# Optimization experiments

Measured on AMD Instinct MI355X. Metric: run time of the kernel, lower is better.

Reference implementation:

```python
import jax, jax.numpy as jnp
import numpy as np

MARGIN = 0.3
EPS = 1e-12


def setup_inputs() -> dict:
    key = jax.random.key(0)
    k1, k2, k3, k4 = jax.random.split(key, 4)
    B, N, D = 4, 6400, 32
    pred_masks = jax.random.normal(k1, (B, N, D), dtype=jnp.float32)
    pos_rand = jax.random.uniform(k2, (B, N), dtype=jnp.float32)
    target_gt_idx = jax.random.randint(k3, (B, N), 0, 20, dtype=jnp.int64)
    fg_mask = jax.random.randint(k4, (B, N), 0, 2) > 0
    return {
        "pred_masks": pred_masks,
        "pos_rand": pos_rand,
        "target_gt_idx": target_gt_idx,
        "fg_mask": fg_mask,
    }


def reference(pred_masks, pos_rand, target_gt_idx, fg_mask):
    B, N, D = pred_masks.shape
    # L2-normalize coefficients (F.normalize, eps=1e-12)
    norm = jnp.sqrt(jnp.sum(pred_masks * pred_masks, axis=-1, keepdims=True))
    coeffs = pred_masks / jnp.maximum(norm, EPS)  # [B,N,D]

    valid_pair = fg_mask[:, :, None] & fg_mask[:, None, :]  # [B,N,N]
    same_inst = target_gt_idx[:, :, None] == target_gt_idx[:, None, :]
    eye = jnp.eye(N, dtype=bool)
    S = valid_pair & same_inst & ~eye          # positives (same instance, not self)
    Dm = valid_pair & ~same_inst               # negatives (different instance)

    # Cosine similarities (vectors are unit norm)
    sims = jnp.einsum('bnd,bmd->bnm', coeffs, coeffs)  # [B,N,N]

    # Hardest negative per anchor: argmax similarity among negatives
    neg_idx = jnp.argmax(jnp.where(Dm, sims, -jnp.inf), axis=-1)  # [B,N]
    neg_vec = jnp.take_along_axis(coeffs, neg_idx[..., None], axis=1)  # [B,N,D]

    # Random positive: pick the k-th positive in anchor order, k = floor(u*num_pos)
    num_pos = jnp.sum(S, axis=-1)  # [B,N]
    pos_choice = jnp.floor(pos_rand * num_pos.astype(pos_rand.dtype)).astype(jnp.int32)
    pos_choice = jnp.clip(pos_choice, 0, jnp.maximum(num_pos - 1, 0).astype(jnp.int32))
    cum = jnp.cumsum(S.astype(jnp.int32), axis=-1)  # rank of each positive
    sel = S & (cum == (pos_choice + 1)[..., None])  # one-hot over chosen positive
    pos_idx = jnp.argmax(sel, axis=-1)  # [B,N]
    pos_vec = jnp.take_along_axis(coeffs, pos_idx[..., None], axis=1)  # [B,N,D]

    pos_d = jnp.sqrt(jnp.sum((coeffs - pos_vec) ** 2, axis=-1) + EPS)
    neg_d = jnp.sqrt(jnp.sum((coeffs - neg_vec) ** 2, axis=-1) + EPS)

    valid = fg_mask & (num_pos >= 1) & jnp.any(Dm, axis=-1)  # anchor forms a triplet
    per_anchor = jnp.maximum(pos_d - neg_d + MARGIN, 0.0)
    n_trip = jnp.sum(valid)
    total = jnp.sum(per_anchor * valid.astype(per_anchor.dtype))
    return jnp.where(n_trip > 0, total / jnp.maximum(n_trip, 1).astype(total.dtype), 0.0)
```

## Files before the change

### kernel.cpp

```cpp
#include <hip/hip_runtime.h>
#include <math.h>

#define B_ 4
#define N_ 6400
#define D_ 32
#define TJ 256
#define NCHJ 25
#define TI 128
#define CHUNK 256
#define NCC 25

typedef __attribute__((ext_vector_type(4))) float f32x4;
typedef __attribute__((ext_vector_type(8))) short bf16x8;

static constexpr float MARGIN_ = 0.3f;

__device__ __forceinline__ unsigned fmap(float f) {
    unsigned u = __float_as_uint(f);
    return (u & 0x80000000u) ? ~u : (u | 0x80000000u);
}
__device__ __forceinline__ float funmap(unsigned u) {
    return (u & 0x80000000u) ? __uint_as_float(u ^ 0x80000000u)
                             : __uint_as_float(~u);
}
#define NEG_INF_MAPPED 0x007FFFFFu

__device__ __forceinline__ unsigned short f2bf(float f) {
    unsigned u = __float_as_uint(f);
    unsigned r = u + 0x7fffu + ((u >> 16) & 1u);
    return (unsigned short)(r >> 16);
}
__device__ __forceinline__ float bf2f(unsigned short h) {
    return __uint_as_float(((unsigned)h) << 16);
}
__device__ __forceinline__ void bf2x(unsigned u, float& e0, float& e1) {
    e0 = __uint_as_float(u << 16);
    e1 = __uint_as_float(u & 0xffff0000u);
}

__global__ __launch_bounds__(256) void k_prep(const float* __restrict__ pred,
                                              const int* __restrict__ gt,
                                              const int* __restrict__ fg,
                                              unsigned short* __restrict__ hi_g,
                                              unsigned short* __restrict__ lo_g,
                                              int* __restrict__ clist,
                                              int* __restrict__ cg,
                                              int* __restrict__ Marr,
                                              unsigned* __restrict__ bestArr) {
    int c = blockIdx.x, b = blockIdx.y;
    int t = threadIdx.x;
    int lane = t & 63, w = t >> 6;
    int idx = c * CHUNK + t;

    bestArr[b * N_ + idx] = NEG_INF_MAPPED;

    bool flag = fg[b * N_ + idx] != 0;
    unsigned long long m = __ballot(flag);
    int lp = __popcll(m & ((1ull << lane) - 1ull));
    __shared__ int wsh[4];
    __shared__ int s_off, s_M;
    if (lane == 0) wsh[w] = __popcll(m);

    if (w == 0) {
        int pre = 0, tot = 0;
        #pragma unroll
        for (int cc = 0; cc < NCC; ++cc) {
            const int4 v = ((const int4*)(fg + (size_t)b * N_ + cc * CHUNK))[lane];
            int cnt = (v.x != 0) + (v.y != 0) + (v.z != 0) + (v.w != 0);
            #pragma unroll
            for (int o = 1; o < 64; o <<= 1) cnt += __shfl_xor(cnt, o);
            pre += (cc < c) ? cnt : 0;
            tot += cnt;
        }
        if (lane == 0) { s_off = pre; s_M = tot; }
    }
    __syncthreads();
    if (c == 0 && t == 0) Marr[b] = s_M;
    if (!flag) return;

    int woff = 0;
    #pragma unroll
    for (int k = 0; k < 4; ++k) if (k < w) woff += wsh[k];
    int rank = s_off + woff + lp;
    clist[b * N_ + rank] = idx;
    cg[b * N_ + rank] = gt[b * N_ + idx];

    const float4* s4 = (const float4*)(pred + ((size_t)b * N_ + idx) * D_);
    float f[32];
    float ssq = 0.0f;
    #pragma unroll
    for (int k = 0; k < 8; ++k) {
        float4 q = s4[k];
        f[k * 4] = q.x; f[k * 4 + 1] = q.y; f[k * 4 + 2] = q.z; f[k * 4 + 3] = q.w;
        ssq += q.x * q.x + q.y * q.y + q.z * q.z + q.w * q.w;
    }
    float inv = 1.0f / fmaxf(sqrtf(ssq), 1e-12f);
    unsigned hw[16], lw[16];
    #pragma unroll
    for (int k = 0; k < 16; ++k) {
        float x0 = f[2 * k] * inv, x1 = f[2 * k + 1] * inv;
        unsigned short h0 = f2bf(x0), h1 = f2bf(x1);
        unsigned short l0 = f2bf(x0 - bf2f(h0)), l1 = f2bf(x1 - bf2f(h1));
        hw[k] = (unsigned)h0 | ((unsigned)h1 << 16);
        lw[k] = (unsigned)l0 | ((unsigned)l1 << 16);
    }
    uint4* dh = (uint4*)(hi_g + ((size_t)b * N_ + rank) * 32);
    uint4* dl = (uint4*)(lo_g + ((size_t)b * N_ + rank) * 32);
    #pragma unroll
    for (int k = 0; k < 4; ++k) {
        dh[k] = make_uint4(hw[4 * k], hw[4 * k + 1], hw[4 * k + 2], hw[4 * k + 3]);
        dl[k] = make_uint4(lw[4 * k], lw[4 * k + 1], lw[4 * k + 2], lw[4 * k + 3]);
    }
}

__global__ __launch_bounds__(256) void k_pass(const unsigned short* __restrict__ hi_g,
                                              const unsigned short* __restrict__ lo_g,
                                              const int* __restrict__ cg,
                                              const int* __restrict__ Marr,
                                              unsigned short* __restrict__ p_cnt,
                                              unsigned* __restrict__ bestArr) {
    int b = blockIdx.z;
    int M = Marr[b];
    int i0 = blockIdx.x * TI;
    int j0 = blockIdx.y * TJ;
    if (i0 >= M || j0 >= M) return;

    __shared__ __align__(16) unsigned short sc_hi[TJ * 40];
    __shared__ __align__(16) unsigned short sc_lo[TJ * 40];
    __shared__ int sg[TJ];
    int t = threadIdx.x;

    {
        int j = j0 + t;
        sg[t] = (j < M) ? cg[b * N_ + j] : -1;
    }
    {
        int seg = t & 3, r0 = t >> 2;
        #pragma unroll
        for (int p = 0; p < 4; ++p) {
            int row = p * 64 + r0;
            int j = j0 + row;
            uint4 vh = make_uint4(0u, 0u, 0u, 0u), vl = make_uint4(0u, 0u, 0u, 0u);
            if (j < M) {
                vh = *(const uint4*)(hi_g + ((size_t)b * N_ + j) * 32 + seg * 8);
                vl = *(const uint4*)(lo_g + ((size_t)b * N_ + j) * 32 + seg * 8);
            }
            *(uint4*)(sc_hi + row * 40 + seg * 8) = vh;
            *(uint4*)(sc_lo + row * 40 + seg * 8) = vl;
        }
    }
    __syncthreads();

    int lane = t & 63, w = t >> 6;
    int r = lane & 15, quad = lane >> 4;
    int ib = i0 + w * 32;

    bf16x8 a_hi[2], a_lo[2];
    int gt_i[2][4];
    #pragma unroll
    for (int it = 0; it < 2; ++it) {
        int i = ib + it * 16 + r;
        bf16x8 zh = {0, 0, 0, 0, 0, 0, 0, 0};
        a_hi[it] = zh; a_lo[it] = zh;
        if (i < M) {
            a_hi[it] = *(const bf16x8*)(hi_g + ((size_t)b * N_ + i) * 32 + quad * 8);
            a_lo[it] = *(const bf16x8*)(lo_g + ((size_t)b * N_ + i) * 32 + quad * 8);
        }
        #pragma unroll
        for (int r4 = 0; r4 < 4; ++r4) {
            int ia = ib + it * 16 + quad * 4 + r4;
            gt_i[it][r4] = (ia < M) ? cg[b * N_ + ia] : -2;
        }
    }

    float best[2][4];
    int cnt[2][4];
    #pragma unroll
    for (int it = 0; it < 2; ++it)
        #pragma unroll
        for (int r4 = 0; r4 < 4; ++r4) { best[it][r4] = -INFINITY; cnt[it][r4] = 0; }

    int jrows = min(TJ, M - j0);
    int ntile = (jrows + 15) >> 4;
    for (int jt = 0; jt < ntile; ++jt) {
        int gtj = sg[jt * 16 + r];
        bf16x8 bh = *(const bf16x8*)(sc_hi + (jt * 16 + r) * 40 + quad * 8);
        bf16x8 bl = *(const bf16x8*)(sc_lo + (jt * 16 + r) * 40 + quad * 8);
        bool jv = (gtj >= 0);
        #pragma unroll
        for (int it = 0; it < 2; ++it) {
            f32x4 acc = {0.f, 0.f, 0.f, 0.f};
            acc = __builtin_amdgcn_mfma_f32_16x16x32_bf16(a_hi[it], bh, acc, 0, 0, 0);
            acc = __builtin_amdgcn_mfma_f32_16x16x32_bf16(a_hi[it], bl, acc, 0, 0, 0);
            acc = __builtin_amdgcn_mfma_f32_16x16x32_bf16(a_lo[it], bh, acc, 0, 0, 0);
            #pragma unroll
            for (int r4 = 0; r4 < 4; ++r4) {
                float s = acc[r4];
                bool same = (gtj == gt_i[it][r4]);
                float sm = (same || !jv) ? -INFINITY : s;
                best[it][r4] = fmaxf(best[it][r4], sm);
                cnt[it][r4] += same ? 1 : 0;
            }
        }
    }

    #pragma unroll
    for (int it = 0; it < 2; ++it) {
        #pragma unroll
        for (int r4 = 0; r4 < 4; ++r4) {
            float bb = best[it][r4];
            int cc = cnt[it][r4];
            #pragma unroll
            for (int mk = 1; mk < 16; mk <<= 1) {
                bb = fmaxf(bb, __shfl_xor(bb, mk));
                cc += __shfl_xor(cc, mk);
            }
            if (r == 0) {
                int ia = ib + it * 16 + quad * 4 + r4;
                if (ia < M) {
                    p_cnt[((size_t)b * N_ + ia) * NCHJ + blockIdx.y] = (unsigned short)cc;
                    if (bb > -INFINITY) atomicMax(&bestArr[b * N_ + ia], fmap(bb));
                }
            }
        }
    }
}

__global__ __launch_bounds__(256) void k_combine(const unsigned short* __restrict__ hi_g,
                                                 const unsigned short* __restrict__ lo_g,
                                                 const int* __restrict__ cg,
                                                 const int* __restrict__ clist,
                                                 const int* __restrict__ Marr,
                                                 const float* __restrict__ pos_rand,
                                                 const unsigned short* __restrict__ p_cnt,
                                                 const unsigned* __restrict__ bestArr,
                                                 float* __restrict__ cArr,
                                                 int* __restrict__ vArr) {
    int b = blockIdx.y;
    int M = Marr[b];
    int t = threadIdx.x;
    int w = t >> 6, lane = t & 63;
    int i = blockIdx.x * 4 + w;

    if (i >= M) return;

    float contrib = 0.0f;
    int vflag = 0;

    int nchj = (M + TJ - 1) / TJ;
    int ich = i / TJ;
    const unsigned short* pc = p_cnt + ((size_t)b * N_ + i) * NCHJ;
    int c_s = 0;
    if (lane < nchj) c_s = (int)pc[lane] - (lane == ich ? 1 : 0);
    int P = c_s;
    #pragma unroll
    for (int off = 1; off < 64; off <<= 1) {
        int n = __shfl_up(P, off);
        if (lane >= off) P += n;
    }
    int num_pos = __shfl(P, 63);
    unsigned bu = bestArr[b * N_ + i];
    if (num_pos >= 1 && bu != NEG_INF_MAPPED) {
        float best = funmap(bu);
        int orig = clist[b * N_ + i];
        float u = pos_rand[b * N_ + orig];
        int pcx = (int)floorf(u * (float)num_pos);
        int hi2 = num_pos - 1;
        pcx = pcx < 0 ? 0 : (pcx > hi2 ? hi2 : pcx);
        int target = pcx + 1;
        unsigned long long selm = __ballot(P >= target);
        int sstar = __ffsll((unsigned long long)selm) - 1;
        int c0 = (sstar > 0) ? __shfl(P, sstar - 1) : 0;
        int need = target - c0;
        int jstart = sstar * TJ;
        int jend = min(jstart + TJ, M);
        int ga = cg[b * N_ + i];
        int posj = -1;
        #pragma unroll
        for (int k = 0; k < 4; ++k) {
            if (posj >= 0) continue;
            int j = jstart + k * 64 + lane;
            bool flag = (j < jend) && (cg[b * N_ + j] == ga) && (j != i);
            unsigned long long mk = __ballot(flag);
            int tot = __popcll(mk);
            if (need <= tot) {
                int pfx = __popcll(mk & ((1ull << lane) - 1ull));
                unsigned long long sel = __ballot(flag && (pfx == need - 1));
                posj = jstart + k * 64 + (__ffsll((unsigned long long)sel) - 1);
            } else {
                need -= tot;
            }
        }
        float part = 0.0f;
        if (lane < 16) {
            unsigned xh = ((const unsigned*)(hi_g + ((size_t)b * N_ + i) * 32))[lane];
            unsigned xl = ((const unsigned*)(lo_g + ((size_t)b * N_ + i) * 32))[lane];
            unsigned yh = ((const unsigned*)(hi_g + ((size_t)b * N_ + posj) * 32))[lane];
            unsigned yl = ((const unsigned*)(lo_g + ((size_t)b * N_ + posj) * 32))[lane];
            float a0, a1, b0, b1, c0f, c1f, d0, d1;
            bf2x(xh, a0, a1); bf2x(xl, b0, b1);
            bf2x(yh, c0f, c1f); bf2x(yl, d0, d1);
            part = fmaf(a0 + b0, c0f + d0, (a1 + b1) * (c1f + d1));
        }
        #pragma unroll
        for (int mk2 = 1; mk2 < 16; mk2 <<= 1) part += __shfl_xor(part, mk2);
        float dot = part;
        float pos_d = sqrtf(fmaxf(2.f - 2.f * dot, 0.f) + 1e-12f);
        float neg_d = sqrtf(fmaxf(2.f - 2.f * best, 0.f) + 1e-12f);
        contrib = fmaxf(pos_d - neg_d + MARGIN_, 0.0f);
        vflag = 1;
    }

    if (lane == 0) {
        cArr[b * N_ + i] = contrib;
        vArr[b * N_ + i] = vflag;
    }
}

__global__ __launch_bounds__(1024) void k_final(const float* __restrict__ cArr,
                                                const int* __restrict__ vArr,
                                                const int* __restrict__ Marr,
                                                float* __restrict__ out) {
    int tid = threadIdx.x;
    float tv = 0.0f;
    int tc = 0;
    #pragma unroll
    for (int b = 0; b < B_; ++b) {
        int M = Marr[b];
        for (int i = tid; i < M; i += 1024) {
            tv += cArr[b * N_ + i];
            tc += vArr[b * N_ + i];
        }
    }
    #pragma unroll
    for (int off = 32; off > 0; off >>= 1) {
        tv += __shfl_down(tv, off);
        tc += __shfl_down(tc, off);
    }
    __shared__ float sv[16];
    __shared__ int scnt[16];
    int lane = tid & 63, w = tid >> 6;
    if (lane == 0) { sv[w] = tv; scnt[w] = tc; }
    __syncthreads();
    if (tid == 0) {
        float T = 0.0f; int C = 0;
        #pragma unroll
        for (int k = 0; k < 16; ++k) { T += sv[k]; C += scnt[k]; }
        out[0] = (C > 0) ? (T / (float)C) : 0.0f;
    }
}

extern "C" void kernel_launch(void* const* d_in, const int* in_sizes, int n_in,
                              void* d_out, int out_size, void* d_ws, size_t ws_size,
                              hipStream_t stream) {
    const float* pred     = (const float*)d_in[0];
    const float* pos_rand = (const float*)d_in[1];
    const int*   gt       = (const int*)d_in[2];
    const int*   fg       = (const int*)d_in[3];
    float* out = (float*)d_out;

    char* ws = (char*)d_ws;
    unsigned short* hi_g    = (unsigned short*)(ws);
    unsigned short* lo_g    = (unsigned short*)(ws + 1638400);
    int*            clist   = (int*)(ws + 3276800);
    int*            cg      = (int*)(ws + 3379200);
    int*            Marr    = (int*)(ws + 3481600);
    unsigned*       bestArr = (unsigned*)(ws + 3482688);
    unsigned short* p_cnt   = (unsigned short*)(ws + 3585088);
    float*          cArr    = (float*)(ws + 4865088);
    int*            vArr    = (int*)(ws + 4967488);

    dim3 gpr(NCC, B_);
    k_prep<<<gpr, 256, 0, stream>>>(pred, gt, fg, hi_g, lo_g, clist, cg, Marr, bestArr);
    dim3 gp((N_ + TI - 1) / TI, (N_ + TJ - 1) / TJ, B_);
    k_pass<<<gp, 256, 0, stream>>>(hi_g, lo_g, cg, Marr, p_cnt, bestArr);
    dim3 gc((N_ + 3) / 4, B_);
    k_combine<<<gc, 256, 0, stream>>>(hi_g, lo_g, cg, clist, Marr, pos_rand, p_cnt, bestArr, cArr, vArr);
    k_final<<<1, 1024, 0, stream>>>(cArr, vArr, Marr, out);
}
```

Baseline: 103.6 us.

## Sort foreground anchors by class to skip same-class tiles and simplify positive selection

The prep kernel now counting-sorts foreground points by instance id (class histogram per chunk plus prefix sums), so each class occupies a contiguous index range. With that layout the pass kernel skips 16-wide tiles that lie entirely inside a single-class anchor group's own range and uses an unmasked max for tiles fully outside it. It also drops the per-chunk positive counting. The combine kernel picks the k-th positive directly as an offset within the class range, and a last-block reduction replaces the separate final kernel. This assumes instance ids lie in [0,20) and that stable within-class ordering matches the reference's anchor order.

```diff
diff --git a/kernel.cpp b/kernel.cpp
--- a/kernel.cpp
+++ b/kernel.cpp
@@ -5,10 +5,12 @@
 #define N_ 6400
 #define D_ 32
 #define TJ 256
-#define NCHJ 25
 #define TI 128
 #define CHUNK 256
 #define NCC 25
+#define NCLS 20
+#define CSROW 24
+#define TOTB (NCC * B_)
 
 typedef __attribute__((ext_vector_type(4))) float f32x4;
 typedef __attribute__((ext_vector_type(8))) short bf16x8;
@@ -36,6 +38,12 @@
 __device__ __forceinline__ void bf2x(unsigned u, float& e0, float& e1) {
     e0 = __uint_as_float(u << 16);
     e1 = __uint_as_float(u & 0xffff0000u);
+}
+__device__ __forceinline__ float dpair(unsigned xh, unsigned xl, unsigned yh, unsigned yl) {
+    float a0, a1, b0, b1, c0, c1, d0, d1;
+    bf2x(xh, a0, a1); bf2x(xl, b0, b1);
+    bf2x(yh, c0, c1); bf2x(yl, d0, d1);
+    return fmaf(a0 + b0, c0 + d0, (a1 + b1) * (c1 + d1));
 }
 
 __global__ __launch_bounds__(256) void k_prep(const float* __restrict__ pred,
@@ -44,46 +52,72 @@
                                               unsigned short* __restrict__ hi_g,
                                               unsigned short* __restrict__ lo_g,
                                               int* __restrict__ clist,
-                                              int* __restrict__ cg,
+                                              int* __restrict__ cgS,
                                               int* __restrict__ Marr,
-                                              unsigned* __restrict__ bestArr) {
+                                              int* __restrict__ csArr,
+                                              unsigned* __restrict__ bestArr,
+                                              unsigned* __restrict__ done) {
     int c = blockIdx.x, b = blockIdx.y;
-    int t = threadIdx.x;
-    int lane = t & 63, w = t >> 6;
+    int t = threadIdx.x, lane = t & 63, w = t >> 6;
     int idx = c * CHUNK + t;
 
     bestArr[b * N_ + idx] = NEG_INF_MAPPED;
+    if (c == 0 && b == 0 && t == 0) *done = 0u;
+
+    __shared__ int cntL[NCC * NCLS];
+    __shared__ int wv[4 * NCLS];
+    __shared__ int totL[NCLS];
+    __shared__ int csL[NCLS + 1];
+    for (int k = t; k < NCC * NCLS; k += 256) cntL[k] = 0;
+    __syncthreads();
+
+    for (int cc = w; cc < NCC; cc += 4) {
+        const int4 f4 = ((const int4*)(fg + (size_t)b * N_ + cc * CHUNK))[lane];
+        const int4 g4 = ((const int4*)(gt + (size_t)b * N_ + cc * CHUNK))[lane];
+        if (f4.x) atomicAdd(&cntL[cc * NCLS + g4.x], 1);
+        if (f4.y) atomicAdd(&cntL[cc * NCLS + g4.y], 1);
+        if (f4.z) atomicAdd(&cntL[cc * NCLS + g4.z], 1);
+        if (f4.w) atomicAdd(&cntL[cc * NCLS + g4.w], 1);
+    }
 
     bool flag = fg[b * N_ + idx] != 0;
-    unsigned long long m = __ballot(flag);
-    int lp = __popcll(m & ((1ull << lane) - 1ull));
-    __shared__ int wsh[4];
-    __shared__ int s_off, s_M;
-    if (lane == 0) wsh[w] = __popcll(m);
-
-    if (w == 0) {
-        int pre = 0, tot = 0;
+    int cls = flag ? gt[b * N_ + idx] : 0;
+    int rnk = 0;
+    unsigned long long below = (1ull << lane) - 1ull;
+    for (int k = 0; k < NCLS; ++k) {
+        unsigned long long m = __ballot(flag && (cls == k));
+        if (flag && cls == k) rnk = __popcll(m & below);
+        if (lane == 0) wv[w * NCLS + k] = __popcll(m);
+    }
+    __syncthreads();
+
+    if (t < NCLS) {
+        int s = 0;
         #pragma unroll
-        for (int cc = 0; cc < NCC; ++cc) {
-            const int4 v = ((const int4*)(fg + (size_t)b * N_ + cc * CHUNK))[lane];
-            int cnt = (v.x != 0) + (v.y != 0) + (v.z != 0) + (v.w != 0);
-            #pragma unroll
-            for (int o = 1; o < 64; o <<= 1) cnt += __shfl_xor(cnt, o);
-            pre += (cc < c) ? cnt : 0;
-            tot += cnt;
-        }
-        if (lane == 0) { s_off = pre; s_M = tot; }
-    }
-    __syncthreads();
-    if (c == 0 && t == 0) Marr[b] = s_M;
+        for (int cc = 0; cc < NCC; ++cc) s += cntL[cc * NCLS + t];
+        totL[t] = s;
+    }
+    __syncthreads();
+    if (t <= NCLS) {
+        int s = 0;
+        for (int k = 0; k < t; ++k) s += totL[k];
+        csL[t] = s;
+    }
+    __syncthreads();
+    if (c == 0) {
+        if (t == 0) Marr[b] = csL[NCLS];
+        if (t <= NCLS) csArr[b * CSROW + t] = csL[t];
+    }
     if (!flag) return;
 
+    int pre = 0;
+    for (int cc = 0; cc < c; ++cc) pre += cntL[cc * NCLS + cls];
     int woff = 0;
     #pragma unroll
-    for (int k = 0; k < 4; ++k) if (k < w) woff += wsh[k];
-    int rank = s_off + woff + lp;
-    clist[b * N_ + rank] = idx;
-    cg[b * N_ + rank] = gt[b * N_ + idx];
+    for (int k = 0; k < 4; ++k) if (k < w) woff += wv[k * NCLS + cls];
+    int dest = csL[cls] + pre + woff + rnk;
+    clist[b * N_ + dest] = idx;
+    cgS[b * N_ + dest] = cls;
 
     const float4* s4 = (const float4*)(pred + ((size_t)b * N_ + idx) * D_);
     float f[32];
@@ -104,8 +138,8 @@
         hw[k] = (unsigned)h0 | ((unsigned)h1 << 16);
         lw[k] = (unsigned)l0 | ((unsigned)l1 << 16);
     }
-    uint4* dh = (uint4*)(hi_g + ((size_t)b * N_ + rank) * 32);
-    uint4* dl = (uint4*)(lo_g + ((size_t)b * N_ + rank) * 32);
+    uint4* dh = (uint4*)(hi_g + ((size_t)b * N_ + dest) * 32);
+    uint4* dl = (uint4*)(lo_g + ((size_t)b * N_ + dest) * 32);
     #pragma unroll
     for (int k = 0; k < 4; ++k) {
         dh[k] = make_uint4(hw[4 * k], hw[4 * k + 1], hw[4 * k + 2], hw[4 * k + 3]);
@@ -115,9 +149,9 @@
 
 __global__ __launch_bounds__(256) void k_pass(const unsigned short* __restrict__ hi_g,
                                               const unsigned short* __restrict__ lo_g,
-                                              const int* __restrict__ cg,
+                                              const int* __restrict__ cgS,
                                               const int* __restrict__ Marr,
-                                              unsigned short* __restrict__ p_cnt,
+                                              const int* __restrict__ csArr,
                                               unsigned* __restrict__ bestArr) {
     int b = blockIdx.z;
     int M = Marr[b];
@@ -132,7 +166,7 @@
 
     {
         int j = j0 + t;
-        sg[t] = (j < M) ? cg[b * N_ + j] : -1;
+        sg[t] = (j < M) ? cgS[b * N_ + j] : -1;
     }
     {
         int seg = t & 3, r0 = t >> 2;
@@ -154,6 +188,7 @@
     int lane = t & 63, w = t >> 6;
     int r = lane & 15, quad = lane >> 4;
     int ib = i0 + w * 32;
+    if (ib >= M) return;
 
     bf16x8 a_hi[2], a_lo[2];
     int gt_i[2][4];
@@ -169,37 +204,60 @@
         #pragma unroll
         for (int r4 = 0; r4 < 4; ++r4) {
             int ia = ib + it * 16 + quad * 4 + r4;
-            gt_i[it][r4] = (ia < M) ? cg[b * N_ + ia] : -2;
-        }
-    }
+            gt_i[it][r4] = (ia < M) ? cgS[b * N_ + ia] : -2;
+        }
+    }
+
+    int ilast = min(ib + 31, M - 1);
+    int cmin = cgS[b * N_ + ib];
+    int cmax = cgS[b * N_ + ilast];
+    int posLo = csArr[b * CSROW + cmin];
+    int posHi = csArr[b * CSROW + cmax + 1];
+    bool oneCls = (cmin == cmax);
 
     float best[2][4];
-    int cnt[2][4];
     #pragma unroll
     for (int it = 0; it < 2; ++it)
         #pragma unroll
-        for (int r4 = 0; r4 < 4; ++r4) { best[it][r4] = -INFINITY; cnt[it][r4] = 0; }
+        for (int r4 = 0; r4 < 4; ++r4) best[it][r4] = -INFINITY;
 
     int jrows = min(TJ, M - j0);
     int ntile = (jrows + 15) >> 4;
     for (int jt = 0; jt < ntile; ++jt) {
-        int gtj = sg[jt * 16 + r];
+        int jlo = j0 + jt * 16;
+        int jvhi = min(jlo + 16, j0 + jrows);
+        if (oneCls && jlo >= posLo && jvhi <= posHi) continue;
+
         bf16x8 bh = *(const bf16x8*)(sc_hi + (jt * 16 + r) * 40 + quad * 8);
         bf16x8 bl = *(const bf16x8*)(sc_lo + (jt * 16 + r) * 40 + quad * 8);
-        bool jv = (gtj >= 0);
-        #pragma unroll
-        for (int it = 0; it < 2; ++it) {
-            f32x4 acc = {0.f, 0.f, 0.f, 0.f};
-            acc = __builtin_amdgcn_mfma_f32_16x16x32_bf16(a_hi[it], bh, acc, 0, 0, 0);
-            acc = __builtin_amdgcn_mfma_f32_16x16x32_bf16(a_hi[it], bl, acc, 0, 0, 0);
-            acc = __builtin_amdgcn_mfma_f32_16x16x32_bf16(a_lo[it], bh, acc, 0, 0, 0);
+        bool full = (jt * 16 + 16) <= jrows;
+
+        if (full && (jlo + 16 <= posLo || jlo >= posHi)) {
             #pragma unroll
-            for (int r4 = 0; r4 < 4; ++r4) {
-                float s = acc[r4];
-                bool same = (gtj == gt_i[it][r4]);
-                float sm = (same || !jv) ? -INFINITY : s;
-                best[it][r4] = fmaxf(best[it][r4], sm);
-                cnt[it][r4] += same ? 1 : 0;
+            for (int it = 0; it < 2; ++it) {
+                f32x4 acc = {0.f, 0.f, 0.f, 0.f};
+                acc = __builtin_amdgcn_mfma_f32_16x16x32_bf16(a_hi[it], bh, acc, 0, 0, 0);
+                acc = __builtin_amdgcn_mfma_f32_16x16x32_bf16(a_hi[it], bl, acc, 0, 0, 0);
+                acc = __builtin_amdgcn_mfma_f32_16x16x32_bf16(a_lo[it], bh, acc, 0, 0, 0);
+                #pragma unroll
+                for (int r4 = 0; r4 < 4; ++r4)
+                    best[it][r4] = fmaxf(best[it][r4], acc[r4]);
+            }
+        } else {
+            int gtj = sg[jt * 16 + r];
+            bool jv = (gtj >= 0);
+            #pragma unroll
+            for (int it = 0; it < 2; ++it) {
+                f32x4 acc = {0.f, 0.f, 0.f, 0.f};
+                acc = __builtin_amdgcn_mfma_f32_16x16x32_bf16(a_hi[it], bh, acc, 0, 0, 0);
+                acc = __builtin_amdgcn_mfma_f32_16x16x32_bf16(a_hi[it], bl, acc, 0, 0, 0);
+                acc = __builtin_amdgcn_mfma_f32_16x16x32_bf16(a_lo[it], bh, acc, 0, 0, 0);
+                #pragma unroll
+                for (int r4 = 0; r4 < 4; ++r4) {
+                    bool same = (gtj == gt_i[it][r4]);
+                    float sm = (same || !jv) ? -INFINITY : acc[r4];
+                    best[it][r4] = fmaxf(best[it][r4], sm);
+                }
             }
         }
     }
@@ -209,18 +267,13 @@
         #pragma unroll
         for (int r4 = 0; r4 < 4; ++r4) {
             float bb = best[it][r4];
-            int cc = cnt[it][r4];
             #pragma unroll
-            for (int mk = 1; mk < 16; mk <<= 1) {
+            for (int mk = 1; mk < 16; mk <<= 1)
                 bb = fmaxf(bb, __shfl_xor(bb, mk));
-                cc += __shfl_xor(cc, mk);
-            }
             if (r == 0) {
                 int ia = ib + it * 16 + quad * 4 + r4;
-                if (ia < M) {
-                    p_cnt[((size_t)b * N_ + ia) * NCHJ + blockIdx.y] = (unsigned short)cc;
-                    if (bb > -INFINITY) atomicMax(&bestArr[b * N_ + ia], fmap(bb));
-                }
+                if (ia < M && bb > -INFINITY)
+                    atomicMax(&bestArr[b * N_ + ia], fmap(bb));
             }
         }
     }
@@ -228,125 +281,94 @@
 
 __global__ __launch_bounds__(256) void k_combine(const unsigned short* __restrict__ hi_g,
                                                  const unsigned short* __restrict__ lo_g,
-                                                 const int* __restrict__ cg,
+                                                 const int* __restrict__ cgS,
                                                  const int* __restrict__ clist,
                                                  const int* __restrict__ Marr,
+                                                 const int* __restrict__ csArr,
                                                  const float* __restrict__ pos_rand,
-                                                 const unsigned short* __restrict__ p_cnt,
                                                  const unsigned* __restrict__ bestArr,
-                                                 float* __restrict__ cArr,
-                                                 int* __restrict__ vArr) {
+                                                 unsigned* __restrict__ partS,
+                                                 unsigned* __restrict__ partC,
+                                                 unsigned* __restrict__ done,
+                                                 float* __restrict__ out) {
     int b = blockIdx.y;
     int M = Marr[b];
-    int t = threadIdx.x;
-    int w = t >> 6, lane = t & 63;
-    int i = blockIdx.x * 4 + w;
-
-    if (i >= M) return;
+    int t = threadIdx.x, lane = t & 63, w = t >> 6;
+    int i = blockIdx.x * 256 + t;
 
     float contrib = 0.0f;
     int vflag = 0;
-
-    int nchj = (M + TJ - 1) / TJ;
-    int ich = i / TJ;
-    const unsigned short* pc = p_cnt + ((size_t)b * N_ + i) * NCHJ;
-    int c_s = 0;
-    if (lane < nchj) c_s = (int)pc[lane] - (lane == ich ? 1 : 0);
-    int P = c_s;
-    #pragma unroll
-    for (int off = 1; off < 64; off <<= 1) {
-        int n = __shfl_up(P, off);
-        if (lane >= off) P += n;
-    }
-    int num_pos = __shfl(P, 63);
-    unsigned bu = bestArr[b * N_ + i];
-    if (num_pos >= 1 && bu != NEG_INF_MAPPED) {
-        float best = funmap(bu);
-        int orig = clist[b * N_ + i];
-        float u = pos_rand[b * N_ + orig];
-        int pcx = (int)floorf(u * (float)num_pos);
-        int hi2 = num_pos - 1;
-        pcx = pcx < 0 ? 0 : (pcx > hi2 ? hi2 : pcx);
-        int target = pcx + 1;
-        unsigned long long selm = __ballot(P >= target);
-        int sstar = __ffsll((unsigned long long)selm) - 1;
-        int c0 = (sstar > 0) ? __shfl(P, sstar - 1) : 0;
-        int need = target - c0;
-        int jstart = sstar * TJ;
-        int jend = min(jstart + TJ, M);
-        int ga = cg[b * N_ + i];
-        int posj = -1;
-        #pragma unroll
-        for (int k = 0; k < 4; ++k) {
-            if (posj >= 0) continue;
-            int j = jstart + k * 64 + lane;
-            bool flag = (j < jend) && (cg[b * N_ + j] == ga) && (j != i);
-            unsigned long long mk = __ballot(flag);
-            int tot = __popcll(mk);
-            if (need <= tot) {
-                int pfx = __popcll(mk & ((1ull << lane) - 1ull));
-                unsigned long long sel = __ballot(flag && (pfx == need - 1));
-                posj = jstart + k * 64 + (__ffsll((unsigned long long)sel) - 1);
-            } else {
-                need -= tot;
-            }
-        }
-        float part = 0.0f;
-        if (lane < 16) {
-            unsigned xh = ((const unsigned*)(hi_g + ((size_t)b * N_ + i) * 32))[lane];
-            unsigned xl = ((const unsigned*)(lo_g + ((size_t)b * N_ + i) * 32))[lane];
-            unsigned yh = ((const unsigned*)(hi_g + ((size_t)b * N_ + posj) * 32))[lane];
-            unsigned yl = ((const unsigned*)(lo_g + ((size_t)b * N_ + posj) * 32))[lane];
-            float a0, a1, b0, b1, c0f, c1f, d0, d1;
-            bf2x(xh, a0, a1); bf2x(xl, b0, b1);
-            bf2x(yh, c0f, c1f); bf2x(yl, d0, d1);
-            part = fmaf(a0 + b0, c0f + d0, (a1 + b1) * (c1f + d1));
-        }
-        #pragma unroll
-        for (int mk2 = 1; mk2 < 16; mk2 <<= 1) part += __shfl_xor(part, mk2);
-        float dot = part;
-        float pos_d = sqrtf(fmaxf(2.f - 2.f * dot, 0.f) + 1e-12f);
-        float neg_d = sqrtf(fmaxf(2.f - 2.f * best, 0.f) + 1e-12f);
-        contrib = fmaxf(pos_d - neg_d + MARGIN_, 0.0f);
-        vflag = 1;
-    }
-
-    if (lane == 0) {
-        cArr[b * N_ + i] = contrib;
-        vArr[b * N_ + i] = vflag;
-    }
-}
-
-__global__ __launch_bounds__(1024) void k_final(const float* __restrict__ cArr,
-                                                const int* __restrict__ vArr,
-                                                const int* __restrict__ Marr,
-                                                float* __restrict__ out) {
-    int tid = threadIdx.x;
-    float tv = 0.0f;
-    int tc = 0;
-    #pragma unroll
-    for (int b = 0; b < B_; ++b) {
-        int M = Marr[b];
-        for (int i = tid; i < M; i += 1024) {
-            tv += cArr[b * N_ + i];
-            tc += vArr[b * N_ + i];
-        }
-    }
+    if (i < M) {
+        int cls = cgS[b * N_ + i];
+        int s0 = csArr[b * CSROW + cls];
+        int s1 = csArr[b * CSROW + cls + 1];
+        int num_pos = s1 - s0 - 1;
+        unsigned bu = bestArr[b * N_ + i];
+        if (num_pos >= 1 && bu != NEG_INF_MAPPED) {
+            float best = funmap(bu);
+            int orig = clist[b * N_ + i];
+            float u = pos_rand[b * N_ + orig];
+            int pcx = (int)floorf(u * (float)num_pos);
+            int hi2 = num_pos - 1;
+            pcx = pcx < 0 ? 0 : (pcx > hi2 ? hi2 : pcx);
+            int ri = i - s0;
+            int posj = s0 + pcx + (pcx >= ri ? 1 : 0);
+
+            const uint4* xh4 = (const uint4*)(hi_g + ((size_t)b * N_ + i) * 32);
+            const uint4* xl4 = (const uint4*)(lo_g + ((size_t)b * N_ + i) * 32);
+            const uint4* yh4 = (const uint4*)(hi_g + ((size_t)b * N_ + posj) * 32);
+            const uint4* yl4 = (const uint4*)(lo_g + ((size_t)b * N_ + posj) * 32);
+            float dot = 0.0f;
+            #pragma unroll
+            for (int q = 0; q < 4; ++q) {
+                uint4 XH = xh4[q], XL = xl4[q], YH = yh4[q], YL = yl4[q];
+                dot += dpair(XH.x, XL.x, YH.x, YL.x);
+                dot += dpair(XH.y, XL.y, YH.y, YL.y);
+                dot += dpair(XH.z, XL.z, YH.z, YL.z);
+                dot += dpair(XH.w, XL.w, YH.w, YL.w);
+            }
+            float pos_d = sqrtf(fmaxf(2.f - 2.f * dot, 0.f) + 1e-12f);
+            float neg_d = sqrtf(fmaxf(2.f - 2.f * best, 0.f) + 1e-12f);
+            contrib = fmaxf(pos_d - neg_d + MARGIN_, 0.0f);
+            vflag = 1;
+        }
+    }
+
     #pragma unroll
     for (int off = 32; off > 0; off >>= 1) {
-        tv += __shfl_down(tv, off);
-        tc += __shfl_down(tc, off);
-    }
-    __shared__ float sv[16];
-    __shared__ int scnt[16];
-    int lane = tid & 63, w = tid >> 6;
-    if (lane == 0) { sv[w] = tv; scnt[w] = tc; }
-    __syncthreads();
-    if (tid == 0) {
-        float T = 0.0f; int C = 0;
-        #pragma unroll
-        for (int k = 0; k < 16; ++k) { T += sv[k]; C += scnt[k]; }
-        out[0] = (C > 0) ? (T / (float)C) : 0.0f;
+        contrib += __shfl_down(contrib, off);
+        vflag += __shfl_down(vflag, off);
+    }
+    __shared__ float ssum[4];
+    __shared__ int scnt[4];
+    if (lane == 0) { ssum[w] = contrib; scnt[w] = vflag; }
+    __syncthreads();
+
+    if (w == 0) {
+        int bid = b * NCC + blockIdx.x;
+        int last = 0;
+        if (lane == 0) {
+            float bs = ssum[0] + ssum[1] + ssum[2] + ssum[3];
+            int bc = scnt[0] + scnt[1] + scnt[2] + scnt[3];
+            atomicExch(&partS[bid], __float_as_uint(bs));
+            atomicExch(&partC[bid], (unsigned)bc);
+            __threadfence();
+            last = (atomicAdd(done, 1u) == (unsigned)(TOTB - 1)) ? 1 : 0;
+        }
+        last = __shfl(last, 0);
+        if (last) {
+            float T = 0.0f; int C = 0;
+            for (int k = lane; k < TOTB; k += 64) {
+                T += __uint_as_float(atomicAdd(&partS[k], 0u));
+                C += (int)atomicAdd(&partC[k], 0u);
+            }
+            #pragma unroll
+            for (int off = 32; off > 0; off >>= 1) {
+                T += __shfl_down(T, off);
+                C += __shfl_down(C, off);
+            }
+            if (lane == 0) out[0] = (C > 0) ? (T / (float)C) : 0.0f;
+        }
     }
 }
 
@@ -363,18 +385,18 @@
     unsigned short* hi_g    = (unsigned short*)(ws);
     unsigned short* lo_g    = (unsigned short*)(ws + 1638400);
     int*            clist   = (int*)(ws + 3276800);
-    int*            cg      = (int*)(ws + 3379200);
+    int*            cgS     = (int*)(ws + 3379200);
     int*            Marr    = (int*)(ws + 3481600);
-    unsigned*       bestArr = (unsigned*)(ws + 3482688);
-    unsigned short* p_cnt   = (unsigned short*)(ws + 3585088);
-    float*          cArr    = (float*)(ws + 4865088);
-    int*            vArr    = (int*)(ws + 4967488);
+    int*            csArr   = (int*)(ws + 3481664);
+    unsigned*       done    = (unsigned*)(ws + 3482048);
+    unsigned*       partS   = (unsigned*)(ws + 3482112);
+    unsigned*       partC   = (unsigned*)(ws + 3482624);
+    unsigned*       bestArr = (unsigned*)(ws + 3483136);
 
     dim3 gpr(NCC, B_);
-    k_prep<<<gpr, 256, 0, stream>>>(pred, gt, fg, hi_g, lo_g, clist, cg, Marr, bestArr);
+    k_prep<<<gpr, 256, 0, stream>>>(pred, gt, fg, hi_g, lo_g, clist, cgS, Marr, csArr, bestArr, done);
     dim3 gp((N_ + TI - 1) / TI, (N_ + TJ - 1) / TJ, B_);
-    k_pass<<<gp, 256, 0, stream>>>(hi_g, lo_g, cg, Marr, p_cnt, bestArr);
-    dim3 gc((N_ + 3) / 4, B_);
-    k_combine<<<gc, 256, 0, stream>>>(hi_g, lo_g, cg, clist, Marr, pos_rand, p_cnt, bestArr, cArr, vArr);
-    k_final<<<1, 1024, 0, stream>>>(cArr, vArr, Marr, out);
-}
+    k_pass<<<gp, 256, 0, stream>>>(hi_g, lo_g, cgS, Marr, csArr, bestArr);
+    dim3 gc(NCC, B_);
+    k_combine<<<gc, 256, 0, stream>>>(hi_g, lo_g, cgS, clist, Marr, csArr, pos_rand, bestArr, partS, partC, done, out);
+}
```

Result: faster. 98.96 us (-4.5%).
